# Kernel optimization log

Hardware: AMD Instinct MI355X
Metric: run time of the kernel (lower is better)

## Reference

```python
import jax, jax.numpy as jnp
import numpy as np

N = 20000      # nodes
E = 320000     # edges
F_IN = 64      # input_dim
HID = 128      # hidden_dim
H = 2          # heads (hard-coded in BGA)
G = 64         # num graphs (batch_step_dim[0])
MID = 32       # middle_dim
OUT = 1        # output_dim
EPS = 1e-5


def setup_inputs() -> dict:
    key = jax.random.key(0)
    ks = jax.random.split(key, 24)
    p = lambda k, shape: jax.random.normal(k, shape, jnp.float32) * 0.05
    inp = {}
    inp["x"] = jax.random.normal(ks[0], (N, F_IN), jnp.float32)
    inp["edge_index"] = jax.random.randint(ks[1], (2, E), 0, N)
    inp["atten_edge_index"] = jax.random.randint(ks[2], (2, E), 0, N)
    inp["batch_index"] = jnp.sort(jax.random.randint(ks[3], (N,), 0, G))
    # GANConv 0 MLP (2-layer: Linear->BN->ReLU->Linear)
    inp["g0_w1"] = p(ks[4], (F_IN, HID)); inp["g0_b1"] = jnp.zeros((HID,), jnp.float32)
    inp["g0_bn_g"] = jnp.ones((HID,), jnp.float32); inp["g0_bn_b"] = jnp.zeros((HID,), jnp.float32)
    inp["g0_w2"] = p(ks[5], (HID, HID)); inp["g0_b2"] = jnp.zeros((HID,), jnp.float32)
    # GANConv 1 MLP
    inp["g1_w1"] = p(ks[6], (HID, HID)); inp["g1_b1"] = jnp.zeros((HID,), jnp.float32)
    inp["g1_bn_g"] = jnp.ones((HID,), jnp.float32); inp["g1_bn_b"] = jnp.zeros((HID,), jnp.float32)
    inp["g1_w2"] = p(ks[7], (HID, HID)); inp["g1_b2"] = jnp.zeros((HID,), jnp.float32)
    # BGA batch norms after each GANConv
    inp["bn0_g"] = jnp.ones((HID,), jnp.float32); inp["bn0_b"] = jnp.zeros((HID,), jnp.float32)
    inp["bn1_g"] = jnp.ones((HID,), jnp.float32); inp["bn1_b"] = jnp.zeros((HID,), jnp.float32)
    # ATTConv atten_self: in=HID, out=HID, heads=2, concat=True
    inp["a1_wl"] = p(ks[8], (HID, H * HID)); inp["a1_bl"] = jnp.zeros((H * HID,), jnp.float32)
    inp["a1_wr"] = p(ks[9], (HID, H * HID)); inp["a1_br"] = jnp.zeros((H * HID,), jnp.float32)
    inp["a1_att"] = p(ks[10], (H, HID))
    inp["a1_bias"] = jnp.zeros((H * HID,), jnp.float32)
    # ATTConv atten: in=H*HID, out=HID, heads=2, concat=False (mean over heads)
    inp["a2_wl"] = p(ks[11], (H * HID, H * HID)); inp["a2_bl"] = jnp.zeros((H * HID,), jnp.float32)
    inp["a2_wr"] = p(ks[12], (H * HID, H * HID)); inp["a2_br"] = jnp.zeros((H * HID,), jnp.float32)
    inp["a2_att"] = p(ks[13], (H, HID))
    inp["a2_bias"] = jnp.zeros((HID,), jnp.float32)
    # prediction heads (only layer 0 and last are used)
    inp["pred0_w"] = p(ks[14], (F_IN, MID)); inp["pred0_b"] = jnp.zeros((MID,), jnp.float32)
    inp["predL_w"] = p(ks[15], (HID, MID)); inp["predL_b"] = jnp.zeros((MID,), jnp.float32)
    inp["out_w"] = p(ks[16], (MID, OUT)); inp["out_b"] = jnp.zeros((OUT,), jnp.float32)
    return inp


def _bn(x, g, b):  # training-mode batch norm over node axis
    m = x.mean(0)
    v = x.var(0)
    return (x - m) * jax.lax.rsqrt(v + EPS) * g + b


def _mlp2(x, w1, b1, bn_g, bn_b, w2, b2):
    h = jax.nn.relu(_bn(x @ w1 + b1, bn_g, bn_b))
    return h @ w2 + b2


def _gan_conv(x, edge_index, w1, b1, bn_g, bn_b, w2, b2):
    row, col = edge_index[0], edge_index[1]
    agg = jax.ops.segment_sum(x[col], row, num_segments=x.shape[0])
    return _mlp2(x + agg, w1, b1, bn_g, bn_b, w2, b2)


def _att_conv(x, edge_index, wl, bl, wr, br, att, bias, concat):
    # GATv2-style: e = leaky_relu(x_i + x_j); alpha = softmax_dst(<e, att>)
    n = x.shape[0]
    xl = (x @ wl + bl).reshape(n, H, HID)  # source proj
    xr = (x @ wr + br).reshape(n, H, HID)  # target proj
    src, dst = edge_index[0], edge_index[1]
    e = jax.nn.leaky_relu(xl[src] + xr[dst], 0.2)          # [E,H,C]
    logit = jnp.einsum('ehc,hc->eh', e, att)               # [E,H]
    lmax = jax.ops.segment_max(logit, dst, num_segments=n)
    w = jnp.exp(logit - lmax[dst])
    denom = jax.ops.segment_sum(w, dst, num_segments=n)
    alpha = w / (denom[dst] + 1e-16)                       # [E,H]
    out = jax.ops.segment_sum(xl[src] * alpha[:, :, None], dst, num_segments=n)
    if concat:
        out = out.reshape(n, H * HID)
    else:
        out = out.mean(1)
    return out + bias, alpha


def reference(x, edge_index, atten_edge_index, batch_index,
              g0_w1, g0_b1, g0_bn_g, g0_bn_b, g0_w2, g0_b2,
              g1_w1, g1_b1, g1_bn_g, g1_bn_b, g1_w2, g1_b2,
              bn0_g, bn0_b, bn1_g, bn1_b,
              a1_wl, a1_bl, a1_wr, a1_br, a1_att, a1_bias,
              a2_wl, a2_bl, a2_wr, a2_br, a2_att, a2_bias,
              pred0_w, pred0_b, predL_w, predL_b, out_w, out_b):
    h0 = x
    h1 = jax.nn.relu(_bn(_gan_conv(h0, edge_index, g0_w1, g0_b1, g0_bn_g, g0_bn_b, g0_w2, g0_b2), bn0_g, bn0_b))
    h2 = jax.nn.relu(_bn(_gan_conv(h1, edge_index, g1_w1, g1_b1, g1_bn_g, g1_bn_b, g1_w2, g1_b2), bn1_g, bn1_b))
    emb, _ = _att_conv(h2, edge_index, a1_wl, a1_bl, a1_wr, a1_br, a1_att, a1_bias, concat=True)
    emb = jax.nn.relu(emb)
    atten_out, alpha = _att_conv(emb, atten_edge_index, a2_wl, a2_bl, a2_wr, a2_br, a2_att, a2_bias, concat=False)
    atten_out = jax.nn.relu(atten_out)
    pool0 = jax.ops.segment_sum(h0, batch_index, num_segments=G)
    poolL = jax.ops.segment_sum(atten_out, batch_index, num_segments=G)
    out_h = jax.nn.relu((pool0 @ pred0_w + pred0_b) + (poolL @ predL_w + predL_b))
    outputs = out_h @ out_w + out_b
    return (outputs, atten_out, alpha)
```

## Files before the change

### kernel.cpp

```cpp
#include <hip/hip_runtime.h>
#include <hip/hip_bf16.h>

#define N_NODES 20000
#define E_EDGES 320000
#define F_INN   64
#define HID     128
#define HEADS   2
#define HC      (HEADS * HID)
#define G_GR    64
#define MIDD    32
#define EPSV    1e-5f
#define NBUK    79

#define CDIV(a, b) (((a) + (b) - 1) / (b))

typedef __attribute__((ext_vector_type(8))) short          bf16x8;
typedef __attribute__((ext_vector_type(4))) float          f32x4;
typedef __attribute__((ext_vector_type(8))) unsigned short u16x8;

__device__ inline float bf2f(unsigned short u) { return __uint_as_float((unsigned)u << 16); }
__device__ inline unsigned short f2bf(float f) {
    unsigned u = __float_as_uint(f);
    unsigned r = u + 0x7FFFu + ((u >> 16) & 1u);
    return (unsigned short)(r >> 16);
}

struct Csr3 {
    const int* key[3];
    const int* other[3];
    int* btot;
    int* bstart;
    int* bcur;
    int* rowptr[3];
    int* out[3];
    int2* tmp;
};

__global__ __launch_bounds__(256) void k_bhist(Csr3 c) {
    __shared__ int hist[NBUK];
    const int y = blockIdx.y;
    const int chunk0 = blockIdx.x * 4096;
    const int t = threadIdx.x;
    for (int i = t; i < NBUK; i += 256) hist[i] = 0;
    __syncthreads();
#pragma unroll
    for (int i = 0; i < 16; i++) {
        int e = chunk0 + (i << 8) + t;
        if (e < E_EDGES) atomicAdd(&hist[c.key[y][e] >> 8], 1);
    }
    __syncthreads();
    for (int i = t; i < NBUK; i += 256)
        if (hist[i] > 0) atomicAdd(&c.btot[y * NBUK + i], hist[i]);
}

__global__ void k_bscan(Csr3 c) {
    __shared__ int sh[3 * NBUK];
    int t = threadIdx.x;
    for (int i = t; i < 3 * NBUK; i += 256) sh[i] = c.btot[i];
    __syncthreads();
    if (t < 3) {
        int run = 0;
        int* bs = c.bstart + t * (NBUK + 1);
        for (int b = 0; b < NBUK; b++) {
            bs[b] = run;
            c.bcur[t * NBUK + b] = run;
            run += sh[t * NBUK + b];
        }
        bs[NBUK] = run;
    }
}

__global__ __launch_bounds__(256) void k_bucketA(Csr3 c) {
    __shared__ int hist[NBUK], base[NBUK], off[NBUK];
    const int y = blockIdx.y;
    const int chunk0 = blockIdx.x * 4096;
    const int t = threadIdx.x;
    for (int i = t; i < NBUK; i += 256) { hist[i] = 0; off[i] = 0; }
    __syncthreads();
    int keys[16], vals[16], bks[16];
#pragma unroll
    for (int i = 0; i < 16; i++) {
        int e = chunk0 + (i << 8) + t;
        bool ok = (e < E_EDGES);
        int k = ok ? c.key[y][e] : 0;
        keys[i] = k;
        vals[i] = ok ? ((y == 2) ? e : c.other[y][e]) : 0;
        bks[i] = ok ? (k >> 8) : -1;
        if (ok) atomicAdd(&hist[k >> 8], 1);
    }
    __syncthreads();
    if (t < NBUK && hist[t] > 0) base[t] = atomicAdd(&c.bcur[y * NBUK + t], hist[t]);
    __syncthreads();
    int2* ty = c.tmp + (size_t)y * E_EDGES;
#pragma unroll
    for (int i = 0; i < 16; i++) {
        int b = bks[i];
        if (b >= 0) {
            int o = atomicAdd(&off[b], 1);
            ty[base[b] + o] = make_int2(keys[i], vals[i]);
        }
    }
}

__global__ __launch_bounds__(256) void k_bucketB(Csr3 c) {
    __shared__ int cnt[256], lbase[256], run[256];
    const int y = blockIdx.y;
    const int b = blockIdx.x;
    const int nbase = b << 8;
    const int t = threadIdx.x;
    cnt[t] = 0; run[t] = 0;
    __syncthreads();
    const int bs = c.bstart[y * (NBUK + 1) + b];
    const int be = c.bstart[y * (NBUK + 1) + b + 1];
    const int2* ty = c.tmp + (size_t)y * E_EDGES;
    for (int i = bs + t; i < be; i += 256)
        atomicAdd(&cnt[ty[i].x - nbase], 1);
    __syncthreads();
    int v = cnt[t];
    lbase[t] = v;
    __syncthreads();
    for (int off = 1; off < 256; off <<= 1) {
        int u = (t >= off) ? lbase[t - off] : 0;
        __syncthreads();
        lbase[t] += u;
        __syncthreads();
    }
    int excl = lbase[t] - v;
    __syncthreads();
    lbase[t] = excl;
    __syncthreads();
    int n = nbase + t;
    if (n < N_NODES) c.rowptr[y][n] = bs + excl;
    if (b == NBUK - 1 && t == 0) c.rowptr[y][N_NODES] = E_EDGES;
    int* outy = c.out[y];
    for (int i = bs + t; i < be; i += 256) {
        int2 kv = ty[i];
        int k = kv.x - nbase;
        int o = atomicAdd(&run[k], 1);
        outy[bs + lbase[k] + o] = kv.y;
    }
}

__global__ __launch_bounds__(256) void k_gather_f32(const float4* __restrict__ x,
                                                    const int* __restrict__ rowptr,
                                                    const int* __restrict__ srcs,
                                                    unsigned short* __restrict__ z) {
    int gid = blockIdx.x * blockDim.x + threadIdx.x;
    int n = gid >> 4;
    if (n >= N_NODES) return;
    int q = gid & 15;
    float4 acc = x[((size_t)n << 4) + q];
    float4 a1 = make_float4(0.f, 0.f, 0.f, 0.f), a2 = a1, a3 = a1;
    int p = rowptr[n], p1 = rowptr[n + 1];
    for (; p + 4 <= p1; p += 4) {
        float4 v0 = x[((size_t)srcs[p + 0] << 4) + q];
        float4 v1 = x[((size_t)srcs[p + 1] << 4) + q];
        float4 v2 = x[((size_t)srcs[p + 2] << 4) + q];
        float4 v3 = x[((size_t)srcs[p + 3] << 4) + q];
        acc.x += v0.x; acc.y += v0.y; acc.z += v0.z; acc.w += v0.w;
        a1.x += v1.x; a1.y += v1.y; a1.z += v1.z; a1.w += v1.w;
        a2.x += v2.x; a2.y += v2.y; a2.z += v2.z; a2.w += v2.w;
        a3.x += v3.x; a3.y += v3.y; a3.z += v3.z; a3.w += v3.w;
    }
    for (; p < p1; p++) {
        float4 v = x[((size_t)srcs[p] << 4) + q];
        acc.x += v.x; acc.y += v.y; acc.z += v.z; acc.w += v.w;
    }
    acc.x += a1.x + a2.x + a3.x; acc.y += a1.y + a2.y + a3.y;
    acc.z += a1.z + a2.z + a3.z; acc.w += a1.w + a2.w + a3.w;
    ushort4 o;
    o.x = f2bf(acc.x); o.y = f2bf(acc.y); o.z = f2bf(acc.z); o.w = f2bf(acc.w);
    *(ushort4*)&z[((size_t)n << 6) + (q << 2)] = o;
}

__global__ __launch_bounds__(256) void k_gather_bn(const u16x8* __restrict__ raw,
                                                   const int* __restrict__ rowptr,
                                                   const int* __restrict__ srcs,
                                                   const float* __restrict__ bn_sums,
                                                   const float* __restrict__ g,
                                                   const float* __restrict__ b,
                                                   u16x8* __restrict__ z) {
    int gid = blockIdx.x * blockDim.x + threadIdx.x;
    int n = gid >> 4;
    if (n >= N_NODES) return;
    int q = gid & 15;
    float sc[8], sh[8];
#pragma unroll
    for (int i = 0; i < 8; i++) {
        int c = (q << 3) + i;
        float mean = bn_sums[c] / N_NODES;
        float istd = rsqrtf(bn_sums[HID + c] / N_NODES - mean * mean + EPSV);
        float s = istd * g[c];
        sc[i] = s;
        sh[i] = b[c] - mean * s;
    }
    u16x8 u0 = raw[((size_t)n << 4) + q];
    float acc[8];
#pragma unroll
    for (int i = 0; i < 8; i++) acc[i] = fmaxf(bf2f(u0[i]) * sc[i] + sh[i], 0.f);
    int p = rowptr[n], p1 = rowptr[n + 1];
    for (; p + 4 <= p1; p += 4) {
        u16x8 v0 = raw[((size_t)srcs[p + 0] << 4) + q];
        u16x8 v1 = raw[((size_t)srcs[p + 1] << 4) + q];
        u16x8 v2 = raw[((size_t)srcs[p + 2] << 4) + q];
        u16x8 v3 = raw[((size_t)srcs[p + 3] << 4) + q];
#pragma unroll
        for (int i = 0; i < 8; i++) {
            acc[i] += fmaxf(bf2f(v0[i]) * sc[i] + sh[i], 0.f)
                    + fmaxf(bf2f(v1[i]) * sc[i] + sh[i], 0.f)
                    + fmaxf(bf2f(v2[i]) * sc[i] + sh[i], 0.f)
                    + fmaxf(bf2f(v3[i]) * sc[i] + sh[i], 0.f);
        }
    }
    for (; p < p1; p++) {
        u16x8 v = raw[((size_t)srcs[p] << 4) + q];
#pragma unroll
        for (int i = 0; i < 8; i++) acc[i] += fmaxf(bf2f(v[i]) * sc[i] + sh[i], 0.f);
    }
    u16x8 o;
#pragma unroll
    for (int i = 0; i < 8; i++) o[i] = f2bf(acc[i]);
    z[((size_t)n << 4) + q] = o;
}

struct WtJob  { const float* src; unsigned short* dst; int K; int N; };
struct WtJobs { WtJob j[8]; };
__global__ void k_wt_cast(WtJobs jobs) {
    WtJob jb = jobs.j[blockIdx.y];
    int total = jb.K * jb.N;
    for (int i = blockIdx.x * blockDim.x + threadIdx.x; i < total; i += gridDim.x * blockDim.x) {
        int nn = i / jb.K, kk = i - nn * jb.K;
        jb.dst[i] = f2bf(jb.src[(size_t)kk * jb.N + nn]);
    }
}

template <int STATS, int BNA, int TM, int BIAS2>
__global__ __launch_bounds__(256) void k_mfma_gemm(const unsigned short* __restrict__ A,
                                                   const unsigned short* __restrict__ Wt,
                                                   const float* __restrict__ biasL,
                                                   const float* __restrict__ biasR,
                                                   unsigned short* __restrict__ Cout,
                                                   int M, int K, int N,
                                                   float* __restrict__ stats_sums,
                                                   const float* __restrict__ bn_sums,
                                                   const float* __restrict__ bn_g,
                                                   const float* __restrict__ bn_b) {
    constexpr int BNF = (TM == 128) ? 4 : 2;
    __shared__ unsigned short As[TM][40];
    __shared__ unsigned short Bs[128][40];
    __shared__ float s_scale[BNA ? HID : 1], s_shift[BNA ? HID : 1];
    const int t = threadIdx.x;
    if (BNA) {
        if (t < HID) {
            float mean = bn_sums[t] / M;
            float istd = rsqrtf(bn_sums[HID + t] / M - mean * mean + EPSV);
            float s = istd * bn_g[t];
            s_scale[t] = s;
            s_shift[t] = bn_b[t] - mean * s;
        }
        __syncthreads();
    }
    const int wave = t >> 6, lane = t & 63;
    const int row0 = blockIdx.y * TM, col0 = blockIdx.x * 128;
    const int wm = (TM == 128) ? ((wave & 1) << 6) : 0;
    const int wn = (TM == 128) ? ((wave >> 1) << 6) : (wave << 5);
    const int lm = lane & 15, lk = (lane >> 4) << 3;
    constexpr int APASS = TM / 64;
    f32x4 acc[4][BNF] = {};
    for (int k0 = 0; k0 < K; k0 += 32) {
        u16x8 av[APASS], wv[2];
#pragma unroll
        for (int i = 0; i < APASS; i++) {
            int c = t + (i << 8);
            int r = c >> 2, ko = (c & 3) << 3;
            u16x8 zv = {};
            int gr = row0 + r;
            av[i] = (gr < M) ? *(const u16x8*)&A[(size_t)gr * K + k0 + ko] : zv;
            if (BNA) {
#pragma unroll
                for (int j = 0; j < 8; j++) {
                    int kc = k0 + ko + j;
                    float v = fmaxf(bf2f(av[i][j]) * s_scale[kc] + s_shift[kc], 0.f);
                    av[i][j] = f2bf(v);
                }
            }
        }
#pragma unroll
        for (int i = 0; i < 2; i++) {
            int c = t + (i << 8);
            int r = c >> 2, ko = (c & 3) << 3;
            wv[i] = *(const u16x8*)&Wt[(size_t)(col0 + r) * K + k0 + ko];
        }
        __syncthreads();
#pragma unroll
        for (int i = 0; i < APASS; i++) {
            int c = t + (i << 8);
            int r = c >> 2, ko = (c & 3) << 3;
            *(u16x8*)&As[r][ko] = av[i];
        }
#pragma unroll
        for (int i = 0; i < 2; i++) {
            int c = t + (i << 8);
            int r = c >> 2, ko = (c & 3) << 3;
            *(u16x8*)&Bs[r][ko] = wv[i];
        }
        __syncthreads();
        bf16x8 af[4], bfm[BNF];
#pragma unroll
        for (int i = 0; i < 4; i++) af[i]  = *(const bf16x8*)&As[wm + (i << 4) + lm][lk];
#pragma unroll
        for (int j = 0; j < BNF; j++) bfm[j] = *(const bf16x8*)&Bs[wn + (j << 4) + lm][lk];
#pragma unroll
        for (int i = 0; i < 4; i++)
#pragma unroll
            for (int j = 0; j < BNF; j++)
                acc[i][j] = __builtin_amdgcn_mfma_f32_16x16x32_bf16(af[i], bfm[j], acc[i][j], 0, 0, 0);
    }
    const int lr4 = (lane >> 4) << 2;
    float s1[BNF], s2[BNF];
#pragma unroll
    for (int j = 0; j < BNF; j++) { s1[j] = 0.f; s2[j] = 0.f; }
#pragma unroll
    for (int j = 0; j < BNF; j++) {
        int col = col0 + wn + (j << 4) + lm;
        float bv = BIAS2 ? ((col < 256) ? biasL[col] : biasR[col - 256]) : biasL[col];
#pragma unroll
        for (int i = 0; i < 4; i++) {
#pragma unroll
            for (int r = 0; r < 4; r++) {
                int row = row0 + wm + (i << 4) + lr4 + r;
                if (row < M) {
                    float v = acc[i][j][r] + bv;
                    Cout[(size_t)row * N + col] = f2bf(v);
                    if (STATS) { s1[j] += v; s2[j] += v * v; }
                }
            }
        }
    }
    if (STATS) {
#pragma unroll
        for (int j = 0; j < BNF; j++) {
            s1[j] += __shfl_xor(s1[j], 16, 64); s1[j] += __shfl_xor(s1[j], 32, 64);
            s2[j] += __shfl_xor(s2[j], 16, 64); s2[j] += __shfl_xor(s2[j], 32, 64);
        }
        if ((lane >> 4) == 0) {
#pragma unroll
            for (int j = 0; j < BNF; j++) {
                int col = col0 + wn + (j << 4) + lm;
                atomicAdd(&stats_sums[col], s1[j]);
                atomicAdd(&stats_sums[HID + col], s2[j]);
            }
        }
    }
}

#define ATT_CAP 192
template <int CONCAT, int WITH_ALPHA>
__global__ __launch_bounds__(256) void k_att_fused(const ushort4* __restrict__ Q,
                                                   const int* __restrict__ rowptr,
                                                   const int* __restrict__ plist,
                                                   const int* __restrict__ other,
                                                   const float* __restrict__ att,
                                                   const float* __restrict__ bias,
                                                   void* __restrict__ outp,
                                                   float* __restrict__ alpha_out) {
    __shared__ float s_lg[WITH_ALPHA ? 4 : 1][WITH_ALPHA ? ATT_CAP : 1][2];
    const int t = threadIdx.x;
    const int wave = t >> 6, l = t & 63;
    const int n = blockIdx.x * 4 + wave;
    const int h = l >> 5;
    ushort4 ur = Q[((size_t)n << 7) + 64 + l];
    float xr4[4] = {bf2f(ur.x), bf2f(ur.y), bf2f(ur.z), bf2f(ur.w)};
    const float* ap = &att[h * HID + ((l & 31) << 2)];
    float at4[4] = {ap[0], ap[1], ap[2], ap[3]};
    const int p0 = rowptr[n], p1 = rowptr[n + 1];

    float m = -INFINITY, ssum = 0.f;
    float acc[4] = {0.f, 0.f, 0.f, 0.f};

#define ATT_SRC(p) (WITH_ALPHA ? other[plist[p]] : plist[p])

#define ATT_LOGIT(uv, x4, tl) do { \
        x4[0] = bf2f(uv.x); x4[1] = bf2f(uv.y); x4[2] = bf2f(uv.z); x4[3] = bf2f(uv.w); \
        float v0 = x4[0] + xr4[0]; v0 = (v0 > 0.f) ? v0 : 0.2f * v0; \
        float v1 = x4[1] + xr4[1]; v1 = (v1 > 0.f) ? v1 : 0.2f * v1; \
        float v2 = x4[2] + xr4[2]; v2 = (v2 > 0.f) ? v2 : 0.2f * v2; \
        float v3 = x4[3] + xr4[3]; v3 = (v3 > 0.f) ? v3 : 0.2f * v3; \
        tl = at4[0] * v0 + at4[1] * v1 + at4[2] * v2 + at4[3] * v3; \
    } while (0)

#define ATT_ONLINE(x4, tl, idx) do { \
        float mn = fmaxf(m, tl); \
        float sc = __expf(m - mn); \
        float w  = __expf(tl - mn); \
        ssum = ssum * sc + w; \
        acc[0] = acc[0] * sc + w * x4[0]; \
        acc[1] = acc[1] * sc + w * x4[1]; \
        acc[2] = acc[2] * sc + w * x4[2]; \
        acc[3] = acc[3] * sc + w * x4[3]; \
        m = mn; \
        if (WITH_ALPHA && (idx) < ATT_CAP && (l & 31) == 0) s_lg[wave][idx][h] = tl; \
    } while (0)

    int p = p0;
    for (; p + 4 <= p1; p += 4) {
        float x4[4][4], tl[4];
        ushort4 uv[4];
        int ss[4];
#pragma unroll
        for (int j = 0; j < 4; j++) ss[j] = ATT_SRC(p + j);
#pragma unroll
        for (int j = 0; j < 4; j++) uv[j] = Q[((size_t)ss[j] << 7) + l];
#pragma unroll
        for (int j = 0; j < 4; j++) ATT_LOGIT(uv[j], x4[j], tl[j]);
#pragma unroll
        for (int k = 1; k <= 16; k <<= 1) {
#pragma unroll
            for (int j = 0; j < 4; j++) tl[j] += __shfl_xor(tl[j], k, 64);
        }
#pragma unroll
        for (int j = 0; j < 4; j++) ATT_ONLINE(x4[j], tl[j], p + j - p0);
    }
    for (; p < p1; p++) {
        float x4[4], tl;
        ushort4 uv = Q[((size_t)ATT_SRC(p) << 7) + l];
        ATT_LOGIT(uv, x4, tl);
#pragma unroll
        for (int k = 1; k <= 16; k <<= 1) tl += __shfl_xor(tl, k, 64);
        ATT_ONLINE(x4, tl, p - p0);
    }
    float inv = 1.f / (ssum + 1e-16f);

    if (WITH_ALPHA) {
        float m_o   = __shfl_xor(m, 32, 64);
        float inv_o = __shfl_xor(inv, 32, 64);
        float m2[2], i2[2];
        m2[h] = m; m2[1 - h] = m_o;
        i2[h] = inv; i2[1 - h] = inv_o;
        int cnt = p1 - p0;
        int ccnt = (cnt < ATT_CAP) ? cnt : ATT_CAP;
        for (int i = l; i < ccnt * 2; i += 64) {
            int idx = i >> 1, hh = i & 1;
            float a = __expf(s_lg[wave][idx][hh] - m2[hh]) * i2[hh];
            alpha_out[plist[p0 + idx] * HEADS + hh] = a;
        }
        for (int pp = p0 + ATT_CAP; pp < p1; pp++) {
            float x4[4], tl;
            ushort4 uv = Q[((size_t)ATT_SRC(pp) << 7) + l];
            ATT_LOGIT(uv, x4, tl);
#pragma unroll
            for (int k = 1; k <= 16; k <<= 1) tl += __shfl_xor(tl, k, 64);
            if ((l & 31) == 0) alpha_out[plist[pp] * HEADS + h] = __expf(tl - m) * inv;
        }
    }

    if (CONCAT) {
        const float* bp = &bias[l << 2];
        ushort4 o;
        o.x = f2bf(fmaxf(acc[0] * inv + bp[0], 0.f));
        o.y = f2bf(fmaxf(acc[1] * inv + bp[1], 0.f));
        o.z = f2bf(fmaxf(acc[2] * inv + bp[2], 0.f));
        o.w = f2bf(fmaxf(acc[3] * inv + bp[3], 0.f));
        ((ushort4*)outp)[((size_t)n << 6) + l] = o;
    } else {
        float o[4];
#pragma unroll
        for (int i = 0; i < 4; i++) {
            float v = acc[i] * inv;
            float other_v = __shfl_xor(v, 32, 64);
            o[i] = 0.5f * (v + other_v);
        }
        if (l < 32) {
            const float* bp = &bias[(l & 31) << 2];
            float4 ov;
            ov.x = fmaxf(o[0] + bp[0], 0.f); ov.y = fmaxf(o[1] + bp[1], 0.f);
            ov.z = fmaxf(o[2] + bp[2], 0.f); ov.w = fmaxf(o[3] + bp[3], 0.f);
            ((float4*)outp)[((size_t)n << 5) + l] = ov;
        }
    }
#undef ATT_SRC
#undef ATT_LOGIT
#undef ATT_ONLINE
}

template <int C>
__global__ __launch_bounds__(256) void k_pool_atomic(const float* __restrict__ X,
                                                     const int* __restrict__ batch,
                                                     float* __restrict__ pool, int npb) {
    const int RP = 256 / C;
    int c = threadIdx.x & (C - 1);
    int rofs = threadIdx.x / C;
    int i0 = blockIdx.x * npb;
    int i1 = min(i0 + npb, N_NODES);
    float acc = 0.f;
    int gcur = -1;
    for (int i = i0 + rofs; i < i1; i += RP) {
        int g = batch[i];
        if (g != gcur) {
            if (gcur >= 0) atomicAdd(&pool[gcur * C + c], acc);
            acc = 0.f; gcur = g;
        }
        acc += X[(size_t)i * C + c];
    }
    if (gcur >= 0) atomicAdd(&pool[gcur * C + c], acc);
}

__global__ void k_head(const float* __restrict__ pool0, const float* __restrict__ poolL,
                       const float* __restrict__ p0w, const float* __restrict__ p0b,
                       const float* __restrict__ pLw, const float* __restrict__ pLb,
                       const float* __restrict__ ow, const float* __restrict__ ob,
                       float* __restrict__ outputs) {
    int g = blockIdx.x;
    int m = threadIdx.x;
    __shared__ float sh[MIDD];
    if (m < MIDD) {
        float s = p0b[m] + pLb[m];
        for (int k = 0; k < F_INN; k++) s += pool0[g * F_INN + k] * p0w[k * MIDD + m];
        for (int k = 0; k < HID; k++)  s += poolL[g * HID + k] * pLw[k * MIDD + m];
        sh[m] = fmaxf(s, 0.f);
    }
    __syncthreads();
    if (m == 0) {
        float s = ob[0];
        for (int k = 0; k < MIDD; k++) s += sh[k] * ow[k];
        outputs[g] = s;
    }
}

extern "C" void kernel_launch(void* const* d_in, const int* in_sizes, int n_in,
                              void* d_out, int out_size, void* d_ws, size_t ws_size,
                              hipStream_t stream) {
    const float* x      = (const float*)d_in[0];
    const int*   ei     = (const int*)d_in[1];
    const int*   aei    = (const int*)d_in[2];
    const int*   batch  = (const int*)d_in[3];
    const float* g0_w1  = (const float*)d_in[4];
    const float* g0_b1  = (const float*)d_in[5];
    const float* g0_bng = (const float*)d_in[6];
    const float* g0_bnb = (const float*)d_in[7];
    const float* g0_w2  = (const float*)d_in[8];
    const float* g0_b2  = (const float*)d_in[9];
    const float* g1_w1  = (const float*)d_in[10];
    const float* g1_b1  = (const float*)d_in[11];
    const float* g1_bng = (const float*)d_in[12];
    const float* g1_bnb = (const float*)d_in[13];
    const float* g1_w2  = (const float*)d_in[14];
    const float* g1_b2  = (const float*)d_in[15];
    const float* bn0_g  = (const float*)d_in[16];
    const float* bn0_b  = (const float*)d_in[17];
    const float* bn1_g  = (const float*)d_in[18];
    const float* bn1_b  = (const float*)d_in[19];
    const float* a1_wl  = (const float*)d_in[20];
    const float* a1_bl  = (const float*)d_in[21];
    const float* a1_wr  = (const float*)d_in[22];
    const float* a1_br  = (const float*)d_in[23];
    const float* a1_att = (const float*)d_in[24];
    const float* a1_bias= (const float*)d_in[25];
    const float* a2_wl  = (const float*)d_in[26];
    const float* a2_bl  = (const float*)d_in[27];
    const float* a2_wr  = (const float*)d_in[28];
    const float* a2_br  = (const float*)d_in[29];
    const float* a2_att = (const float*)d_in[30];
    const float* a2_bias= (const float*)d_in[31];
    const float* p0w    = (const float*)d_in[32];
    const float* p0b    = (const float*)d_in[33];
    const float* pLw    = (const float*)d_in[34];
    const float* pLb    = (const float*)d_in[35];
    const float* ow     = (const float*)d_in[36];
    const float* ob     = (const float*)d_in[37];

    float* out_head  = (float*)d_out;
    float* atten_out = out_head + G_GR;
    float* alpha_out = atten_out + (size_t)N_NODES * HID;

    float* ws = (float*)d_ws;
    float* sums4 = ws;
    float* pool0 = sums4 + 4 * 256;
    float* poolL = pool0 + G_GR * F_INN;
    int*   btot  = (int*)(poolL + G_GR * HID);
    const size_t zero_bytes = (4 * 256 + G_GR * F_INN + G_GR * HID + 3 * NBUK) * 4;

    int* ip = btot + 3 * NBUK;
    int* bstart = ip; ip += 3 * (NBUK + 1);
    int* bcur   = ip; ip += 3 * NBUK;
    int* rowptr[3]; int* payload[3];
    for (int c = 0; c < 3; c++) {
        rowptr[c]  = ip; ip += N_NODES + 1;
        payload[c] = ip; ip += E_EDGES;
    }
    int2* tmp3 = (int2*)ip; ip += 2 * 3 * E_EDGES;
    const size_t NB = (size_t)N_NODES * HC;
    unsigned short* B1 = (unsigned short*)ip;
    unsigned short* B2 = B1 + NB;
    unsigned short* Qb = B2 + NB;
    unsigned short* g0w1t = Qb + 2 * NB;
    unsigned short* g0w2t = g0w1t + 128 * 64;
    unsigned short* g1w1t = g0w2t + 128 * 128;
    unsigned short* g1w2t = g1w1t + 128 * 128;
    unsigned short* a1wlt = g1w2t + 128 * 128;
    unsigned short* a1wrt = a1wlt + 256 * 128;
    unsigned short* a2wlt = a1wrt + 256 * 128;
    unsigned short* a2wrt = a2wlt + 256 * 256;

    const int* e_row = ei;
    const int* e_col = ei + E_EDGES;
    const int* a_src = aei;
    const int* a_dst = aei + E_EDGES;

    const int TB = 256;
#define GRID1(n) dim3(CDIV((n), TB))

    {
        WtJobs jobs;
        jobs.j[0] = {g0_w1, g0w1t, F_INN, HID};
        jobs.j[1] = {g0_w2, g0w2t, HID,   HID};
        jobs.j[2] = {g1_w1, g1w1t, HID,   HID};
        jobs.j[3] = {g1_w2, g1w2t, HID,   HID};
        jobs.j[4] = {a1_wl, a1wlt, HID,   HC};
        jobs.j[5] = {a1_wr, a1wrt, HID,   HC};
        jobs.j[6] = {a2_wl, a2wlt, HC,    HC};
        jobs.j[7] = {a2_wr, a2wrt, HC,    HC};
        k_wt_cast<<<dim3(32, 8), TB, 0, stream>>>(jobs);
    }

    hipMemsetAsync(sums4, 0, zero_bytes, stream);
    {
        Csr3 c;
        c.key[0] = e_row; c.other[0] = e_col;
        c.key[1] = e_col; c.other[1] = e_row;
        c.key[2] = a_dst; c.other[2] = a_src;
        c.btot = btot; c.bstart = bstart; c.bcur = bcur; c.tmp = tmp3;
        for (int i = 0; i < 3; i++) { c.rowptr[i] = rowptr[i]; c.out[i] = payload[i]; }
        k_bhist<<<dim3(CDIV(E_EDGES, 4096), 3), TB, 0, stream>>>(c);
        k_bscan<<<dim3(1), TB, 0, stream>>>(c);
        k_bucketA<<<dim3(CDIV(E_EDGES, 4096), 3), TB, 0, stream>>>(c);
        k_bucketB<<<dim3(NBUK, 3), TB, 0, stream>>>(c);
    }

    const dim3 gemm_g1(1, CDIV(N_NODES, 64));
    const dim3 gemm_gq(4, CDIV(N_NODES, 128));
    const float* NOF = nullptr;

    k_gather_f32<<<GRID1(N_NODES * 16), TB, 0, stream>>>((const float4*)x, rowptr[0], payload[0], B1);
    k_mfma_gemm<1, 0, 64, 0><<<gemm_g1, TB, 0, stream>>>(B1, g0w1t, g0_b1, NOF, B2, N_NODES, F_INN, HID,
                                                         sums4 + 0, NOF, NOF, NOF);
    k_mfma_gemm<1, 1, 64, 0><<<gemm_g1, TB, 0, stream>>>(B2, g0w2t, g0_b2, NOF, B1, N_NODES, HID, HID,
                                                         sums4 + 256, sums4 + 0, g0_bng, g0_bnb);

    k_gather_bn<<<GRID1(N_NODES * 16), TB, 0, stream>>>((const u16x8*)B1, rowptr[0], payload[0],
                                                        sums4 + 256, bn0_g, bn0_b, (u16x8*)B2);
    k_mfma_gemm<1, 0, 64, 0><<<gemm_g1, TB, 0, stream>>>(B2, g1w1t, g1_b1, NOF, B1, N_NODES, HID, HID,
                                                         sums4 + 512, NOF, NOF, NOF);
    k_mfma_gemm<1, 1, 64, 0><<<gemm_g1, TB, 0, stream>>>(B1, g1w2t, g1_b2, NOF, B2, N_NODES, HID, HID,
                                                         sums4 + 768, sums4 + 512, g1_bng, g1_bnb);

    k_mfma_gemm<0, 1, 128, 1><<<gemm_gq, TB, 0, stream>>>(B2, a1wlt, a1_bl, a1_br, Qb, N_NODES, HID, 512,
                                                          nullptr, sums4 + 768, bn1_g, bn1_b);
    k_att_fused<1, 0><<<dim3(N_NODES / 4), TB, 0, stream>>>(
        (const ushort4*)Qb, rowptr[1], payload[1], nullptr, a1_att, a1_bias, (void*)B1, nullptr);

    k_mfma_gemm<0, 0, 128, 1><<<gemm_gq, TB, 0, stream>>>(B1, a2wlt, a2_bl, a2_br, Qb, N_NODES, HC, 512,
                                                          nullptr, NOF, NOF, NOF);
    k_att_fused<0, 1><<<dim3(N_NODES / 4), TB, 0, stream>>>(
        (const ushort4*)Qb, rowptr[2], payload[2], a_src, a2_att, a2_bias, (void*)atten_out, alpha_out);

    {
        const int npb = 64;
        k_pool_atomic<F_INN><<<dim3(CDIV(N_NODES, npb)), TB, 0, stream>>>(x, batch, pool0, npb);
        k_pool_atomic<HID><<<dim3(CDIV(N_NODES, npb)), TB, 0, stream>>>(atten_out, batch, poolL, npb);
    }
    k_head<<<dim3(G_GR), 64, 0, stream>>>(pool0, poolL, p0w, p0b, pLw, pLb, ow, ob, out_head);
}
```

Measured before the change: 430.7 us.

## Restructure attention kernel: 8-wide loads, two edges per wave, lazy softmax rescale

The fused GAT attention kernel now loads 16-byte vectors (8 bf16) per lane, so each half-wave covers one edge and a wave handles two edges at once. The two halves keep separate online-softmax state and merge it at the end. Rescaling is skipped unless a new logit exceeds the running max by a threshold, and exp is replaced by exp2 on log2e-scaled attention weights. A new pre-gather kernel materializes the source ids in CSR order, removing the double indirection in the second attention layer. This adds an extra launch and a conditional softmax path, and the threshold trick must be numerically safe against overflow.

Result: no change. 428.9 us (-0.4%).

```diff
diff --git a/kernel.cpp b/kernel.cpp
--- a/kernel.cpp
+++ b/kernel.cpp
@@ -25,6 +25,12 @@
     return (unsigned short)(r >> 16);
 }
 
+#if __has_builtin(__builtin_amdgcn_exp2f)
+__device__ inline float fexp2(float x) { return __builtin_amdgcn_exp2f(x); }
+#else
+__device__ inline float fexp2(float x) { return exp2f(x); }
+#endif
+
 struct Csr3 {
     const int* key[3];
     const int* other[3];
@@ -139,6 +145,13 @@
         int o = atomicAdd(&run[k], 1);
         outy[bs + lbase[k] + o] = kv.y;
     }
+}
+
+__global__ __launch_bounds__(256) void k_src_gather(const int* __restrict__ eids,
+                                                    const int* __restrict__ srcs,
+                                                    int* __restrict__ outv) {
+    int i = blockIdx.x * 256 + threadIdx.x;
+    if (i < E_EDGES) outv[i] = srcs[eids[i]];
 }
 
 __global__ __launch_bounds__(256) void k_gather_f32(const float4* __restrict__ x,
@@ -355,11 +368,34 @@
 }
 
 #define ATT_CAP 192
+#define LOG2E   1.4426950408889634f
+#define DTHR    11.0f
+
+__device__ __forceinline__ float att_logit8(u16x8 uv, const float* xr8, const float* at8, float* x8) {
+    float tl = 0.f;
+#pragma unroll
+    for (int i = 0; i < 8; i++) {
+        x8[i] = bf2f(uv[i]);
+        float v = x8[i] + xr8[i];
+        v = (v > 0.f) ? v : 0.2f * v;
+        tl = fmaf(at8[i], v, tl);
+    }
+    return tl;
+}
+
+__device__ __forceinline__ float red16(float tl) {
+    tl += __shfl_xor(tl, 1, 64);
+    tl += __shfl_xor(tl, 2, 64);
+    tl += __shfl_xor(tl, 4, 64);
+    tl += __shfl_xor(tl, 8, 64);
+    return tl;
+}
+
 template <int CONCAT, int WITH_ALPHA>
-__global__ __launch_bounds__(256) void k_att_fused(const ushort4* __restrict__ Q,
+__global__ __launch_bounds__(256) void k_att_fused(const u16x8* __restrict__ Q,
                                                    const int* __restrict__ rowptr,
                                                    const int* __restrict__ plist,
-                                                   const int* __restrict__ other,
+                                                   const int* __restrict__ srclist,
                                                    const float* __restrict__ att,
                                                    const float* __restrict__ bias,
                                                    void* __restrict__ outp,
@@ -368,119 +404,160 @@
     const int t = threadIdx.x;
     const int wave = t >> 6, l = t & 63;
     const int n = blockIdx.x * 4 + wave;
-    const int h = l >> 5;
-    ushort4 ur = Q[((size_t)n << 7) + 64 + l];
-    float xr4[4] = {bf2f(ur.x), bf2f(ur.y), bf2f(ur.z), bf2f(ur.w)};
-    const float* ap = &att[h * HID + ((l & 31) << 2)];
-    float at4[4] = {ap[0], ap[1], ap[2], ap[3]};
+    const int half = l >> 5;
+    const int j = l & 31;
+    const int h = j >> 4;
+
+    u16x8 ur = Q[((size_t)n << 6) + 32 + j];
+    float xr8[8];
+#pragma unroll
+    for (int i = 0; i < 8; i++) xr8[i] = bf2f(ur[i]);
+    const float* ap = &att[h * HID + ((j & 15) << 3)];
+    float at8[8];
+#pragma unroll
+    for (int i = 0; i < 8; i++) at8[i] = ap[i] * LOG2E;
+
     const int p0 = rowptr[n], p1 = rowptr[n + 1];
-
-    float m = -INFINITY, ssum = 0.f;
-    float acc[4] = {0.f, 0.f, 0.f, 0.f};
-
-#define ATT_SRC(p) (WITH_ALPHA ? other[plist[p]] : plist[p])
-
-#define ATT_LOGIT(uv, x4, tl) do { \
-        x4[0] = bf2f(uv.x); x4[1] = bf2f(uv.y); x4[2] = bf2f(uv.z); x4[3] = bf2f(uv.w); \
-        float v0 = x4[0] + xr4[0]; v0 = (v0 > 0.f) ? v0 : 0.2f * v0; \
-        float v1 = x4[1] + xr4[1]; v1 = (v1 > 0.f) ? v1 : 0.2f * v1; \
-        float v2 = x4[2] + xr4[2]; v2 = (v2 > 0.f) ? v2 : 0.2f * v2; \
-        float v3 = x4[3] + xr4[3]; v3 = (v3 > 0.f) ? v3 : 0.2f * v3; \
-        tl = at4[0] * v0 + at4[1] * v1 + at4[2] * v2 + at4[3] * v3; \
-    } while (0)
-
-#define ATT_ONLINE(x4, tl, idx) do { \
-        float mn = fmaxf(m, tl); \
-        float sc = __expf(m - mn); \
-        float w  = __expf(tl - mn); \
-        ssum = ssum * sc + w; \
-        acc[0] = acc[0] * sc + w * x4[0]; \
-        acc[1] = acc[1] * sc + w * x4[1]; \
-        acc[2] = acc[2] * sc + w * x4[2]; \
-        acc[3] = acc[3] * sc + w * x4[3]; \
-        m = mn; \
-        if (WITH_ALPHA && (idx) < ATT_CAP && (l & 31) == 0) s_lg[wave][idx][h] = tl; \
-    } while (0)
+    float m = -1e30f, ssum = 0.f;
+    float acc[8] = {};
+
+#define ATT_SRC(p) (WITH_ALPHA ? srclist[p] : plist[p])
 
     int p = p0;
-    for (; p + 4 <= p1; p += 4) {
-        float x4[4][4], tl[4];
-        ushort4 uv[4];
-        int ss[4];
-#pragma unroll
-        for (int j = 0; j < 4; j++) ss[j] = ATT_SRC(p + j);
-#pragma unroll
-        for (int j = 0; j < 4; j++) uv[j] = Q[((size_t)ss[j] << 7) + l];
-#pragma unroll
-        for (int j = 0; j < 4; j++) ATT_LOGIT(uv[j], x4[j], tl[j]);
-#pragma unroll
-        for (int k = 1; k <= 16; k <<= 1) {
-#pragma unroll
-            for (int j = 0; j < 4; j++) tl[j] += __shfl_xor(tl[j], k, 64);
-        }
-#pragma unroll
-        for (int j = 0; j < 4; j++) ATT_ONLINE(x4[j], tl[j], p + j - p0);
-    }
-    for (; p < p1; p++) {
-        float x4[4], tl;
-        ushort4 uv = Q[((size_t)ATT_SRC(p) << 7) + l];
-        ATT_LOGIT(uv, x4, tl);
-#pragma unroll
-        for (int k = 1; k <= 16; k <<= 1) tl += __shfl_xor(tl, k, 64);
-        ATT_ONLINE(x4, tl, p - p0);
-    }
-    float inv = 1.f / (ssum + 1e-16f);
+    for (; p + 8 <= p1; p += 8) {
+        int s4[4];
+#pragma unroll
+        for (int g = 0; g < 4; g++) s4[g] = ATT_SRC(p + (g << 1) + half);
+        u16x8 uv[4];
+#pragma unroll
+        for (int g = 0; g < 4; g++) uv[g] = Q[((size_t)s4[g] << 6) + j];
+        float x8[4][8], tl[4];
+#pragma unroll
+        for (int g = 0; g < 4; g++) tl[g] = att_logit8(uv[g], xr8, at8, x8[g]);
+#pragma unroll
+        for (int g = 0; g < 4; g++) tl[g] = red16(tl[g]);
+        if (WITH_ALPHA && (j & 15) == 0) {
+#pragma unroll
+            for (int g = 0; g < 4; g++) {
+                int idx = p + (g << 1) + half - p0;
+                if (idx < ATT_CAP) s_lg[wave][idx][h] = tl[g];
+            }
+        }
+        float pm = fmaxf(fmaxf(tl[0], tl[1]), fmaxf(tl[2], tl[3]));
+        if (__builtin_expect(!__all(pm <= m + DTHR), 0)) {
+#pragma unroll
+            for (int g = 0; g < 4; g++) {
+                float mn = fmaxf(m, tl[g]);
+                float sc = fexp2(m - mn);
+                float w  = fexp2(tl[g] - mn);
+                ssum = ssum * sc + w;
+#pragma unroll
+                for (int i = 0; i < 8; i++) acc[i] = acc[i] * sc + w * x8[g][i];
+                m = mn;
+            }
+        } else {
+            float w0 = fexp2(tl[0] - m), w1 = fexp2(tl[1] - m);
+            float w2 = fexp2(tl[2] - m), w3 = fexp2(tl[3] - m);
+            ssum += (w0 + w1) + (w2 + w3);
+#pragma unroll
+            for (int i = 0; i < 8; i++)
+                acc[i] += (w0 * x8[0][i] + w1 * x8[1][i]) + (w2 * x8[2][i] + w3 * x8[3][i]);
+        }
+    }
+    for (; p < p1; p += 2) {
+        const bool v1 = (p + 1 < p1);
+        int sp = (half && v1) ? (p + 1) : p;
+        int src = ATT_SRC(sp);
+        u16x8 uv = Q[((size_t)src << 6) + j];
+        float x8[8], tl;
+        tl = att_logit8(uv, xr8, at8, x8);
+        tl = red16(tl);
+        float vm = (half && !v1) ? 0.f : 1.f;
+        if (vm == 0.f) tl = -1e30f;
+        if (WITH_ALPHA && (j & 15) == 0 && vm != 0.f) {
+            int idx = p + half - p0;
+            if (idx < ATT_CAP) s_lg[wave][idx][h] = tl;
+        }
+        if (__builtin_expect(!__all(tl <= m + DTHR), 0)) {
+            float mn = fmaxf(m, tl);
+            float sc = fexp2(m - mn);
+            float w  = fexp2(tl - mn) * vm;
+            ssum = ssum * sc + w;
+#pragma unroll
+            for (int i = 0; i < 8; i++) acc[i] = acc[i] * sc + w * x8[i];
+            m = mn;
+        } else {
+            float w = fexp2(tl - m) * vm;
+            ssum += w;
+#pragma unroll
+            for (int i = 0; i < 8; i++) acc[i] += w * x8[i];
+        }
+    }
+
+    float m_o = __shfl_xor(m, 32, 64);
+    float mf  = fmaxf(m, m_o);
+    float sA  = fexp2(m - mf);
+    float ssA = ssum * sA;
+    float ssum_f = ssA + __shfl_xor(ssA, 32, 64);
+    float accf[8];
+#pragma unroll
+    for (int i = 0; i < 8; i++) {
+        float a = acc[i] * sA;
+        accf[i] = a + __shfl_xor(a, 32, 64);
+    }
+    float inv = 1.f / (ssum_f + 1e-16f);
 
     if (WITH_ALPHA) {
-        float m_o   = __shfl_xor(m, 32, 64);
-        float inv_o = __shfl_xor(inv, 32, 64);
+        float m_oh   = __shfl_xor(mf, 16, 64);
+        float inv_oh = __shfl_xor(inv, 16, 64);
         float m2[2], i2[2];
-        m2[h] = m; m2[1 - h] = m_o;
-        i2[h] = inv; i2[1 - h] = inv_o;
+        m2[h] = mf;  m2[1 - h] = m_oh;
+        i2[h] = inv; i2[1 - h] = inv_oh;
         int cnt = p1 - p0;
         int ccnt = (cnt < ATT_CAP) ? cnt : ATT_CAP;
         for (int i = l; i < ccnt * 2; i += 64) {
             int idx = i >> 1, hh = i & 1;
-            float a = __expf(s_lg[wave][idx][hh] - m2[hh]) * i2[hh];
+            float a = fexp2(s_lg[wave][idx][hh] - m2[hh]) * i2[hh];
             alpha_out[plist[p0 + idx] * HEADS + hh] = a;
         }
         for (int pp = p0 + ATT_CAP; pp < p1; pp++) {
-            float x4[4], tl;
-            ushort4 uv = Q[((size_t)ATT_SRC(pp) << 7) + l];
-            ATT_LOGIT(uv, x4, tl);
-#pragma unroll
-            for (int k = 1; k <= 16; k <<= 1) tl += __shfl_xor(tl, k, 64);
-            if ((l & 31) == 0) alpha_out[plist[pp] * HEADS + h] = __expf(tl - m) * inv;
+            int src = ATT_SRC(pp);
+            u16x8 uv = Q[((size_t)src << 6) + j];
+            float x8[8], tl;
+            tl = att_logit8(uv, xr8, at8, x8);
+            tl = red16(tl);
+            if ((j & 15) == 0 && half == 0)
+                alpha_out[plist[pp] * HEADS + h] = fexp2(tl - mf) * inv;
         }
     }
 
     if (CONCAT) {
-        const float* bp = &bias[l << 2];
-        ushort4 o;
-        o.x = f2bf(fmaxf(acc[0] * inv + bp[0], 0.f));
-        o.y = f2bf(fmaxf(acc[1] * inv + bp[1], 0.f));
-        o.z = f2bf(fmaxf(acc[2] * inv + bp[2], 0.f));
-        o.w = f2bf(fmaxf(acc[3] * inv + bp[3], 0.f));
-        ((ushort4*)outp)[((size_t)n << 6) + l] = o;
+        if (half == 0) {
+            const float* bp = &bias[j << 3];
+            u16x8 o;
+#pragma unroll
+            for (int i = 0; i < 8; i++) o[i] = f2bf(fmaxf(accf[i] * inv + bp[i], 0.f));
+            ((u16x8*)outp)[((size_t)n << 5) + j] = o;
+        }
     } else {
-        float o[4];
-#pragma unroll
-        for (int i = 0; i < 4; i++) {
-            float v = acc[i] * inv;
-            float other_v = __shfl_xor(v, 32, 64);
-            o[i] = 0.5f * (v + other_v);
-        }
-        if (l < 32) {
-            const float* bp = &bias[(l & 31) << 2];
-            float4 ov;
-            ov.x = fmaxf(o[0] + bp[0], 0.f); ov.y = fmaxf(o[1] + bp[1], 0.f);
-            ov.z = fmaxf(o[2] + bp[2], 0.f); ov.w = fmaxf(o[3] + bp[3], 0.f);
-            ((float4*)outp)[((size_t)n << 5) + l] = ov;
+        float om[8];
+#pragma unroll
+        for (int i = 0; i < 8; i++) {
+            float v = accf[i] * inv;
+            om[i] = 0.5f * (v + __shfl_xor(v, 16, 64));
+        }
+        if (half == 0 && h == 0) {
+            const float* bp = &bias[j << 3];
+            float4 o0, o1;
+            o0.x = fmaxf(om[0] + bp[0], 0.f); o0.y = fmaxf(om[1] + bp[1], 0.f);
+            o0.z = fmaxf(om[2] + bp[2], 0.f); o0.w = fmaxf(om[3] + bp[3], 0.f);
+            o1.x = fmaxf(om[4] + bp[4], 0.f); o1.y = fmaxf(om[5] + bp[5], 0.f);
+            o1.z = fmaxf(om[6] + bp[6], 0.f); o1.w = fmaxf(om[7] + bp[7], 0.f);
+            ((float4*)outp)[((size_t)n << 5) + (j << 1)]     = o0;
+            ((float4*)outp)[((size_t)n << 5) + (j << 1) + 1] = o1;
         }
     }
 #undef ATT_SRC
-#undef ATT_LOGIT
-#undef ATT_ONLINE
 }
 
 template <int C>
@@ -589,6 +666,7 @@
         payload[c] = ip; ip += E_EDGES;
     }
     int2* tmp3 = (int2*)ip; ip += 2 * 3 * E_EDGES;
+    int* srclist = (int*)tmp3;
     const size_t NB = (size_t)N_NODES * HC;
     unsigned short* B1 = (unsigned short*)ip;
     unsigned short* B2 = B1 + NB;
@@ -636,6 +714,7 @@
         k_bucketA<<<dim3(CDIV(E_EDGES, 4096), 3), TB, 0, stream>>>(c);
         k_bucketB<<<dim3(NBUK, 3), TB, 0, stream>>>(c);
     }
+    k_src_gather<<<GRID1(E_EDGES), TB, 0, stream>>>(payload[2], a_src, srclist);
 
     const dim3 gemm_g1(1, CDIV(N_NODES, 64));
     const dim3 gemm_gq(4, CDIV(N_NODES, 128));
@@ -657,12 +736,12 @@
     k_mfma_gemm<0, 1, 128, 1><<<gemm_gq, TB, 0, stream>>>(B2, a1wlt, a1_bl, a1_br, Qb, N_NODES, HID, 512,
                                                           nullptr, sums4 + 768, bn1_g, bn1_b);
     k_att_fused<1, 0><<<dim3(N_NODES / 4), TB, 0, stream>>>(
-        (const ushort4*)Qb, rowptr[1], payload[1], nullptr, a1_att, a1_bias, (void*)B1, nullptr);
+        (const u16x8*)Qb, rowptr[1], payload[1], nullptr, a1_att, a1_bias, (void*)B1, nullptr);
 
     k_mfma_gemm<0, 0, 128, 1><<<gemm_gq, TB, 0, stream>>>(B1, a2wlt, a2_bl, a2_br, Qb, N_NODES, HC, 512,
                                                           nullptr, NOF, NOF, NOF);
     k_att_fused<0, 1><<<dim3(N_NODES / 4), TB, 0, stream>>>(
-        (const ushort4*)Qb, rowptr[2], payload[2], a_src, a2_att, a2_bias, (void*)atten_out, alpha_out);
+        (const u16x8*)Qb, rowptr[2], payload[2], srclist, a2_att, a2_bias, (void*)atten_out, alpha_out);
 
     {
         const int npb = 64;
```
